# Optimization experiments

Measured on AMD Instinct MI355X. Metric: run time of the kernel, lower is better.

The kernel has to match this reference:

```python
import jax, jax.numpy as jnp
import numpy as np

NH = 12  # num_heads


def _rms(y, g, eps=1e-6):
    # RMSNorm over the full model dim (applied before the head reshape, as in the source)
    return y * jax.lax.rsqrt(jnp.mean(y * y, axis=-1, keepdims=True) + eps) * g


def _rope(t, cos, sin, total_len):
    # t: [B, S, n, d]; rotate first total_len tokens, pass the tail through unchanged
    b, s, n, d = t.shape
    c = d // 2
    tm = t[:, :total_len].reshape(b, total_len, n, c, 2)
    tr, ti = tm[..., 0], tm[..., 1]
    co = cos[None, :, None, :]
    si = sin[None, :, None, :]
    rot = jnp.stack([tr * co - ti * si, tr * si + ti * co], axis=-1).reshape(b, total_len, n, d)
    if total_len < s:
        return jnp.concatenate([rot, t[:, total_len:]], axis=1)
    return rot


def setup_inputs() -> dict:
    key = jax.random.key(0)
    ks = jax.random.split(key, 8)
    B, F, H, W = 4, 4, 16, 28
    S = F * H * W  # 1792 tokens
    D = 1536
    d = D // NH    # 128
    c = d // 2     # 64
    MAXSEQ = 64
    x = jax.random.normal(ks[0], (B, S, D), jnp.float32)
    seq_lens = jnp.full((B,), S, dtype=jnp.int32)
    grid_sizes = jnp.tile(jnp.array([[F, H, W]], dtype=jnp.int32), (B, 1))
    ang = jnp.arange(MAXSEQ, dtype=jnp.float32)[:, None] * (
        10000.0 ** (-jnp.arange(c, dtype=jnp.float32) / c))[None, :]
    w = lambda k, shp: jax.random.normal(k, shp, jnp.float32) * 0.02
    return {
        "x": x,
        "seq_lens": seq_lens,
        "grid_sizes": grid_sizes,
        "freqs_cos": jnp.cos(ang),
        "freqs_sin": jnp.sin(ang),
        "Wq": w(ks[1], (D, D)), "bq": jnp.zeros((D,), jnp.float32),
        "Wk": w(ks[2], (D, D)), "bk": jnp.zeros((D,), jnp.float32),
        "Wv": w(ks[3], (D, D)), "bv": jnp.zeros((D,), jnp.float32),
        "Wo": w(ks[4], (D, D)), "bo": jnp.zeros((D,), jnp.float32),
        "gq": jnp.ones((D,), jnp.float32),
        "gk": jnp.ones((D,), jnp.float32),
        "num_modalities": 1,
    }


def reference(x, seq_lens, grid_sizes, freqs_cos, freqs_sin,
              Wq, bq, Wk, bk, Wv, bv, Wo, bo, gq, gk, num_modalities):
    b, s, D = x.shape
    d = D // NH
    c = d // 2
    # QKV projections + RMSNorm on q/k (norm over the full dim, then split heads)
    q = _rms(x @ Wq.T + bq, gq).reshape(b, s, NH, d)
    k = _rms(x @ Wk.T + bk, gk).reshape(b, s, NH, d)
    v = (x @ Wv.T + bv).reshape(b, s, NH, d)
    # grid metadata is static (same grid for all samples in this setup)
    f, h, w = (int(z) for z in np.asarray(grid_sizes)[0])
    m = int(num_modalities)
    ct = c - 2 * (c // 3)
    ch = c // 3
    seq_per = f * h * w
    total_len = min(seq_per * m, s)

    def grid_freqs(fr):
        # build per-token (t,h,w) frequency table: [seq_per, c], tiled over modalities
        ft = jnp.broadcast_to(fr[:f, :ct][:, None, None, :], (f, h, w, ct))
        fh = jnp.broadcast_to(fr[:h, ct:ct + ch][None, :, None, :], (f, h, w, ch))
        fw = jnp.broadcast_to(fr[:w, ct + ch:c][None, None, :, :], (f, h, w, ch))
        base = jnp.concatenate([ft, fh, fw], axis=-1).reshape(seq_per, c)
        return jnp.tile(base, (m, 1))[:total_len]

    cos = grid_freqs(freqs_cos)
    sin = grid_freqs(freqs_sin)
    q = _rope(q, cos, sin, total_len)
    k = _rope(k, cos, sin, total_len)
    # full (window_size=(-1,-1)) attention with k_lens masking
    scale = 1.0 / jnp.sqrt(jnp.float32(d))
    scores = jnp.einsum('bqhd,bkhd->bhqk', q, k) * scale
    kmask = jnp.arange(s)[None, :] < seq_lens[:, None]  # [B, S]
    scores = jnp.where(kmask[:, None, None, :], scores, jnp.float32(-1e30))
    attn = jax.nn.softmax(scores, axis=-1)
    out = jnp.einsum('bhqk,bkhd->bqhd', attn, v).reshape(b, s, D)
    return out @ Wo.T + bo
```

## Files before the change

kernel.cpp:

```cpp
#include <hip/hip_runtime.h>
#include <hip/hip_bf16.h>

typedef short bf16x8 __attribute__((ext_vector_type(8)));
typedef float f32x4 __attribute__((ext_vector_type(4)));
typedef float f32x16 __attribute__((ext_vector_type(16)));

#define NH 12
#define SEQ 1792
#define DMODEL 1536
#define HD 128

static __device__ __forceinline__ void gload16(const void* g, void* l) {
  __builtin_amdgcn_global_load_lds((const __attribute__((address_space(1))) void*)g,
                                   (__attribute__((address_space(3))) void*)l, 16, 0, 0);
}

static __device__ __forceinline__ short f2bf(float x) {
  __hip_bfloat16 h = __float2bfloat16(x);
  return *reinterpret_cast<short*>(&h);
}

static __device__ __forceinline__ unsigned pack2(float lo, float hi) {
  unsigned a = (unsigned)(unsigned short)f2bf(lo);
  unsigned b = (unsigned)(unsigned short)f2bf(hi);
  return a | (b << 16);
}

__global__ __launch_bounds__(256) void cast_all_kernel(
    const float* __restrict__ x, const float* __restrict__ wq, const float* __restrict__ wk,
    const float* __restrict__ wv, const float* __restrict__ wo,
    __hip_bfloat16* __restrict__ xb, __hip_bfloat16* __restrict__ wb,
    __hip_bfloat16* __restrict__ wob) {
  int i = blockIdx.x * 256 + threadIdx.x;
  const float* src; __hip_bfloat16* dst; int j;
  if (i < 2752512)      { src = x;  dst = xb;            j = i; }
  else if (i < 3342336) { src = wq; dst = wb;            j = i - 2752512; }
  else if (i < 3932160) { src = wk; dst = wb + 2359296;  j = i - 3342336; }
  else if (i < 4521984) { src = wv; dst = wb + 4718592;  j = i - 3932160; }
  else if (i < 5111808) { src = wo; dst = wob;           j = i - 4521984; }
  else return;
  float4 v = reinterpret_cast<const float4*>(src)[j];
  short4 r;
  r.x = f2bf(v.x); r.y = f2bf(v.y); r.z = f2bf(v.z); r.w = f2bf(v.w);
  reinterpret_cast<short4*>(dst)[j] = r;
}

template<int MODE>
__global__ __launch_bounds__(512, 2) void gemm8(
    const __hip_bfloat16* __restrict__ A, const __hip_bfloat16* __restrict__ B,
    int nN, int cpx,
    const float* __restrict__ bq, const float* __restrict__ bk, const float* __restrict__ bv,
    __hip_bfloat16* __restrict__ qbuf, __hip_bfloat16* __restrict__ kbuf,
    __hip_bfloat16* __restrict__ vt,
    const float* __restrict__ bo, float* __restrict__ outp)
{
  constexpr int K = DMODEL;
  constexpr int nT = K / 64;
  constexpr int nIt = nT / 2;
  __shared__ __hip_bfloat16 As[2][2][128 * 64];
  __shared__ __hip_bfloat16 Bs[2][2][128 * 64];
  const int tid = threadIdx.x;
  const int l = tid & 63, w = tid >> 6;
  const int lr = l & 15, lg = l >> 4;
  const int wr = w >> 2, wc = w & 3;

  const int orig = blockIdx.x;
  const int wg = (orig & 7) * cpx + (orig >> 3);
  const int m0 = (wg / nN) * 256, n0 = (wg % nN) * 256;

  const int hrow0 = tid >> 3;
  const int scb0 = ((tid & 7) << 4) ^ ((hrow0 & 7) << 4);

  auto stageA = [&](int t, int half) {
    const char* s = (const char*)(A + (size_t)(m0 + half * 128) * K + t * 64);
    char* d = (char*)&As[t & 1][half][0];
    gload16(s + (size_t)hrow0 * (K * 2) + scb0, d + tid * 16);
    gload16(s + (size_t)(hrow0 + 64) * (K * 2) + scb0, d + (tid + 512) * 16);
  };
  auto stageB = [&](int t, int half) {
    const char* s = (const char*)(B + (size_t)(n0 + half * 128) * K + t * 64);
    char* d = (char*)&Bs[t & 1][half][0];
    gload16(s + (size_t)hrow0 * (K * 2) + scb0, d + tid * 16);
    gload16(s + (size_t)(hrow0 + 64) * (K * 2) + scb0, d + (tid + 512) * 16);
  };

  f32x4 acc[8][4] = {};
  bf16x8 afr[4][2], b0f[2][2], b1f[2][2];

  auto rdA = [&](int par, int mh) {
#pragma unroll
    for (int i = 0; i < 4; ++i) {
      int hrow = (mh * 4 + i) * 16 + lr;
#pragma unroll
      for (int ks = 0; ks < 2; ++ks)
        afr[i][ks] = *reinterpret_cast<const bf16x8*>(
            (const char*)&As[par][wr][0] + hrow * 128 +
            ((ks * 64 + lg * 16) ^ ((hrow & 7) << 4)));
    }
  };
  auto rdB = [&](int par, int nh, bf16x8 (&bqf)[2][2]) {
#pragma unroll
    for (int j = 0; j < 2; ++j) {
      int base = wc * 64 + (nh * 2 + j) * 16;
      int half = base >> 7;
      int hrow = (base & 127) + lr;
#pragma unroll
      for (int ks = 0; ks < 2; ++ks)
        bqf[j][ks] = *reinterpret_cast<const bf16x8*>(
            (const char*)&Bs[par][half][0] + hrow * 128 +
            ((ks * 64 + lg * 16) ^ ((hrow & 7) << 4)));
    }
  };
  auto mf = [&](int mh, int nh, bf16x8 (&bqf)[2][2]) {
    __builtin_amdgcn_s_setprio(1);
#pragma unroll
    for (int i = 0; i < 4; ++i)
#pragma unroll
      for (int j = 0; j < 2; ++j)
#pragma unroll
        for (int ks = 0; ks < 2; ++ks)
          acc[mh * 4 + i][nh * 2 + j] = __builtin_amdgcn_mfma_f32_16x16x32_bf16(
              afr[i][ks], bqf[j][ks], acc[mh * 4 + i][nh * 2 + j], 0, 0, 0);
    __builtin_amdgcn_s_setprio(0);
  };

#define LGKM0 do { asm volatile("s_waitcnt lgkmcnt(0)" ::: "memory"); \
                   __builtin_amdgcn_sched_barrier(0); } while (0)
#define BAR __builtin_amdgcn_s_barrier()

  stageA(0, 0); stageA(0, 1); stageB(0, 0); stageB(0, 1); stageA(1, 0);
  asm volatile("s_waitcnt vmcnt(2)" ::: "memory");
  BAR;

  for (int it = 0; it < nIt; ++it) {
    const int t1 = 2 * it + 1, u0 = 2 * it + 2, u1 = 2 * it + 3;
    rdA(0, 0); rdB(0, 0, b0f);
    stageA(t1, 1);
    LGKM0; mf(0, 0, b0f); BAR;
    rdB(0, 1, b1f);
    stageB(t1, 0);
    LGKM0; mf(0, 1, b1f); BAR;
    rdA(0, 1);
    stageB(t1, 1);
    LGKM0; mf(1, 1, b1f); BAR;
    if (u0 < nT) stageA(u0, 0);
    mf(1, 0, b0f);
    if (it + 1 == nIt) asm volatile("s_waitcnt vmcnt(0)" ::: "memory");
    else               asm volatile("s_waitcnt vmcnt(2)" ::: "memory");
    BAR;
    rdA(1, 0); rdB(1, 0, b0f);
    if (u0 < nT) stageA(u0, 1);
    LGKM0; mf(0, 0, b0f); BAR;
    rdB(1, 1, b1f);
    if (u0 < nT) stageB(u0, 0);
    LGKM0; mf(0, 1, b1f); BAR;
    rdA(1, 1);
    if (u0 < nT) stageB(u0, 1);
    LGKM0; mf(1, 1, b1f); BAR;
    if (u1 < nT) stageA(u1, 0);
    mf(1, 0, b0f);
    asm volatile("s_waitcnt vmcnt(2)" ::: "memory");
    BAR;
  }
#undef LGKM0
#undef BAR

  if (MODE == 0) {
#pragma unroll
    for (int fj = 0; fj < 4; ++fj) {
      int ncol = n0 + wc * 64 + fj * 16 + lr;
      int which = ncol / DMODEL;
      int cc = ncol - which * DMODEL;
      int hh = cc >> 7, dd = cc & 127;
      float bias = (which == 0 ? bq : which == 1 ? bk : bv)[cc];
#pragma unroll
      for (int fi = 0; fi < 8; ++fi)
#pragma unroll
        for (int r = 0; r < 4; ++r) {
          int rowg = m0 + wr * 128 + fi * 16 + lg * 4 + r;
          int bbb = rowg / SEQ;
          int sr = rowg - bbb * SEQ;
          __hip_bfloat16 hv = __float2bfloat16(acc[fi][fj][r] + bias);
          if (which == 0)
            qbuf[(((size_t)(bbb * NH + hh)) * SEQ + sr) * HD + dd] = hv;
          else if (which == 1)
            kbuf[(((size_t)(bbb * NH + hh)) * SEQ + sr) * HD + dd] = hv;
          else
            vt[(((size_t)(bbb * NH + hh)) * HD + dd) * SEQ + sr] = hv;
        }
    }
  } else {
#pragma unroll
    for (int fj = 0; fj < 4; ++fj) {
      int ncol = n0 + wc * 64 + fj * 16 + lr;
      float bias = bo[ncol];
#pragma unroll
      for (int fi = 0; fi < 8; ++fi)
#pragma unroll
        for (int r = 0; r < 4; ++r) {
          int rowg = m0 + wr * 128 + fi * 16 + lg * 4 + r;
          outp[(size_t)rowg * DMODEL + ncol] = acc[fi][fj][r] + bias;
        }
    }
  }
}

__global__ __launch_bounds__(256) void rmsrope_kernel(
    __hip_bfloat16* __restrict__ qb, __hip_bfloat16* __restrict__ kb,
    const float* __restrict__ gq, const float* __restrict__ gk,
    const float* __restrict__ fc, const float* __restrict__ fs,
    const int* __restrict__ gsz, const int* __restrict__ nmod)
{
  const int bs = blockIdx.x;
  const int b = bs / SEQ, s = bs - b * SEQ;
  const int t = threadIdx.x;
  const int f = gsz[0], h = gsz[1], wd = gsz[2];
  const int mm = nmod[0];
  const int seq_per = f * h * wd;
  int total_len = seq_per * mm; if (total_len > SEQ) total_len = SEQ;
  const bool dorope = s < total_len;
  int fi = 0, hi2 = 0, wi = 0;
  if (dorope) {
    int p = s % seq_per;
    fi = p / (h * wd);
    int rem = p - fi * (h * wd);
    hi2 = rem / wd;
    wi = rem - hi2 * wd;
  }
  float qv[3][2], kv[3][2];
  float sq = 0.f, sk = 0.f;
#pragma unroll
  for (int r = 0; r < 3; ++r) {
    int pi = t + r * 256;
    int head = pi >> 6;
    int dd = (pi & 63) * 2;
    size_t addr = (((size_t)(b * NH + head)) * SEQ + s) * HD + dd;
    __hip_bfloat162 q2 = *reinterpret_cast<const __hip_bfloat162*>(&qb[addr]);
    __hip_bfloat162 k2 = *reinterpret_cast<const __hip_bfloat162*>(&kb[addr]);
    qv[r][0] = __bfloat162float(q2.x); qv[r][1] = __bfloat162float(q2.y);
    kv[r][0] = __bfloat162float(k2.x); kv[r][1] = __bfloat162float(k2.y);
    sq += qv[r][0] * qv[r][0] + qv[r][1] * qv[r][1];
    sk += kv[r][0] * kv[r][0] + kv[r][1] * kv[r][1];
  }
#pragma unroll
  for (int off = 1; off < 64; off <<= 1) {
    sq += __shfl_xor(sq, off);
    sk += __shfl_xor(sk, off);
  }
  __shared__ float red[2][4];
  if ((t & 63) == 0) { red[0][t >> 6] = sq; red[1][t >> 6] = sk; }
  __syncthreads();
  float tq = red[0][0] + red[0][1] + red[0][2] + red[0][3];
  float tk = red[1][0] + red[1][1] + red[1][2] + red[1][3];
  float rq = rsqrtf(tq * (1.0f / DMODEL) + 1e-6f);
  float rk = rsqrtf(tk * (1.0f / DMODEL) + 1e-6f);
  const float scale = 0.08838834764831845f;
#pragma unroll
  for (int r = 0; r < 3; ++r) {
    int pi = t + r * 256;
    int head = pi >> 6;
    int dd = (pi & 63) * 2;
    int col = pi * 2;
    size_t addr = (((size_t)(b * NH + head)) * SEQ + s) * HD + dd;
    float q0 = qv[r][0] * rq * gq[col], q1 = qv[r][1] * rq * gq[col + 1];
    float k0 = kv[r][0] * rk * gk[col], k1 = kv[r][1] * rk * gk[col + 1];
    if (dorope) {
      int j = pi & 63;
      int row = (j < 22) ? fi : (j < 43) ? hi2 : wi;
      float co = fc[row * 64 + j], si = fs[row * 64 + j];
      float a;
      a = q0 * co - q1 * si; q1 = q0 * si + q1 * co; q0 = a;
      a = k0 * co - k1 * si; k1 = k0 * si + k1 * co; k0 = a;
    }
    q0 *= scale; q1 *= scale;
    __hip_bfloat162 oq, ok;
    oq.x = __float2bfloat16(q0); oq.y = __float2bfloat16(q1);
    ok.x = __float2bfloat16(k0); ok.y = __float2bfloat16(k1);
    *reinterpret_cast<__hip_bfloat162*>(&qb[addr]) = oq;
    *reinterpret_cast<__hip_bfloat162*>(&kb[addr]) = ok;
  }
}

__global__ __launch_bounds__(256, 2) void attn_kernel(
    const __hip_bfloat16* __restrict__ qb, const __hip_bfloat16* __restrict__ kbuf,
    const __hip_bfloat16* __restrict__ vt, const int* __restrict__ seq_lens,
    __hip_bfloat16* __restrict__ ob)
{
  const int orig = blockIdx.x;
  const int wg = (orig & 7) * 84 + (orig >> 3);
  const int bh = wg / 14, qt = wg % 14;
  const int bbb = bh / NH, hh = bh - bbb * NH;
  const int tid = threadIdx.x;
  const int w = tid >> 6, l = tid & 63;
  const int lq = l & 31, h = l >> 5;
  const int sl = seq_lens[bbb];
  const __hip_bfloat16* Q = qb + (size_t)bh * SEQ * HD;
  const char* Kc = (const char*)(kbuf + (size_t)bh * SEQ * HD);
  const __hip_bfloat16* Vp = vt + (size_t)bh * HD * SEQ;
  const int q0 = qt * 128 + w * 32;

  __shared__ __hip_bfloat16 Kt[2][64 * 128];
  __shared__ __hip_bfloat16 Vt[2][128 * 64];

  bf16x8 qf[8];
#pragma unroll
  for (int kc = 0; kc < 8; ++kc)
    qf[kc] = *reinterpret_cast<const bf16x8*>(
        &Q[(size_t)(q0 + lq) * HD + kc * 16 + h * 8]);

  f32x16 oacc[4] = {};
  float m = -3e38f, ll = 0.f;

  const int nkt = (sl + 63) >> 6;

  auto stageK = [&](int buf, int k0) {
    char* Lb = (char*)&Kt[buf][0];
#pragma unroll
    for (int q2 = 0; q2 < 4; ++q2) {
      int chunk = q2 * 256 + tid;
      int row = chunk >> 4;
      int cb = (chunk & 15) << 4;
      int scb = cb ^ ((row & 7) << 4);
      gload16(Kc + (size_t)(k0 + row) * 256 + scb, Lb + chunk * 16);
    }
  };
  auto stageV = [&](int buf, int k0) {
    char* Lb = (char*)&Vt[buf][0];
#pragma unroll
    for (int q2 = 0; q2 < 4; ++q2) {
      int chunk = q2 * 256 + tid;
      int row = chunk >> 3;
      int cb = (chunk & 7) << 4;
      int scb = cb ^ ((row & 7) << 4);
      gload16(Vp + (size_t)row * SEQ + k0 + (scb >> 1), Lb + chunk * 16);
    }
  };

  stageK(0, 0);
  stageV(0, 0);
  for (int kt = 0; kt < nkt; ++kt) {
    __syncthreads();
    const int k0 = kt * 64;
    if (kt + 1 < nkt) { stageK((kt + 1) & 1, k0 + 64); stageV((kt + 1) & 1, k0 + 64); }
    const char* Kl = (const char*)&Kt[kt & 1][0];
    const char* Vl = (const char*)&Vt[kt & 1][0];

    f32x16 sa[2] = {};
#pragma unroll
    for (int cb = 0; cb < 2; ++cb) {
      int row = cb * 32 + lq;
      int swz = (row & 7) << 4;
#pragma unroll
      for (int kc = 0; kc < 8; ++kc) {
        bf16x8 kf = *reinterpret_cast<const bf16x8*>(
            Kl + row * 256 + ((kc * 32 + h * 16) ^ swz));
        sa[cb] = __builtin_amdgcn_mfma_f32_32x32x16_bf16(kf, qf[kc], sa[cb], 0, 0, 0);
      }
    }

    if (k0 + 64 > sl) {
#pragma unroll
      for (int cb = 0; cb < 2; ++cb)
#pragma unroll
        for (int r = 0; r < 16; ++r) {
          int kg = k0 + cb * 32 + (r & 3) + 8 * (r >> 2) + 4 * h;
          if (kg >= sl) sa[cb][r] = -3e38f;
        }
    }

    float mx = -3e38f;
#pragma unroll
    for (int cb = 0; cb < 2; ++cb)
#pragma unroll
      for (int r = 0; r < 16; ++r) mx = fmaxf(mx, sa[cb][r]);
    mx = fmaxf(mx, __shfl_xor(mx, 32));

    if (__any(mx - m > 8.f)) {
      float mn = fmaxf(m, mx);
      float alpha = __expf(m - mn);
      m = mn;
      ll *= alpha;
#pragma unroll
      for (int r = 0; r < 16; ++r) {
        float ar = __shfl(alpha, (r & 3) + 8 * (r >> 2) + 4 * h);
#pragma unroll
        for (int d0 = 0; d0 < 4; ++d0) oacc[d0][r] *= ar;
      }
    }

    float rs = 0.f;
#pragma unroll
    for (int cb = 0; cb < 2; ++cb)
#pragma unroll
      for (int r = 0; r < 16; ++r) {
        float e = __expf(sa[cb][r] - m);
        sa[cb][r] = e;
        rs += e;
      }
    rs += __shfl_xor(rs, 32);
    ll += rs;

#pragma unroll
    for (int c = 0; c < 4; ++c) {
      const int cb = c >> 1, r0 = 8 * (c & 1);
      unsigned A01 = pack2(sa[cb][r0],     sa[cb][r0 + 1]);
      unsigned A23 = pack2(sa[cb][r0 + 2], sa[cb][r0 + 3]);
      unsigned B01 = pack2(sa[cb][r0 + 4], sa[cb][r0 + 5]);
      unsigned B23 = pack2(sa[cb][r0 + 6], sa[cb][r0 + 7]);
      unsigned s1 = __shfl_xor(h ? A01 : B01, 32);
      unsigned s2 = __shfl_xor(h ? A23 : B23, 32);
      int4 wv;
      wv.x = (int)(h ? s1 : A01);
      wv.y = (int)(h ? s2 : A23);
      wv.z = (int)(h ? B01 : s1);
      wv.w = (int)(h ? B23 : s2);
      bf16x8 pa = *reinterpret_cast<bf16x8*>(&wv);
#pragma unroll
      for (int d0 = 0; d0 < 4; ++d0) {
        int vr = d0 * 32 + lq;
        bf16x8 vv = *reinterpret_cast<const bf16x8*>(
            Vl + vr * 128 + ((c * 32 + h * 16) ^ ((vr & 7) << 4)));
        oacc[d0] = __builtin_amdgcn_mfma_f32_32x32x16_bf16(pa, vv, oacc[d0], 0, 0, 0);
      }
    }
  }

  float invl = 1.0f / ll;
#pragma unroll
  for (int r = 0; r < 16; ++r) {
    int qoff = (r & 3) + 8 * (r >> 2) + 4 * h;
    float ir = __shfl(invl, qoff);
    int qrow = q0 + qoff;
#pragma unroll
    for (int d0 = 0; d0 < 4; ++d0)
      ob[((size_t)bbb * SEQ + qrow) * DMODEL + hh * HD + d0 * 32 + lq] =
          __float2bfloat16(oacc[d0][r] * ir);
  }
}

extern "C" void kernel_launch(void* const* d_in, const int* in_sizes, int n_in,
                              void* d_out, int out_size, void* d_ws, size_t ws_size,
                              hipStream_t stream) {
  const float* x   = (const float*)d_in[0];
  const int* seq_lens   = (const int*)d_in[1];
  const int* grid_sizes = (const int*)d_in[2];
  const float* fc  = (const float*)d_in[3];
  const float* fs  = (const float*)d_in[4];
  const float* Wq  = (const float*)d_in[5];
  const float* bq  = (const float*)d_in[6];
  const float* Wk  = (const float*)d_in[7];
  const float* bk  = (const float*)d_in[8];
  const float* Wv  = (const float*)d_in[9];
  const float* bv  = (const float*)d_in[10];
  const float* Wo  = (const float*)d_in[11];
  const float* bo  = (const float*)d_in[12];
  const float* gq  = (const float*)d_in[13];
  const float* gk  = (const float*)d_in[14];
  const int* nmod  = (const int*)d_in[15];
  float* out = (float*)d_out;

  char* ws = (char*)d_ws;
  __hip_bfloat16* xb   = (__hip_bfloat16*)(ws + 0);
  __hip_bfloat16* wb   = (__hip_bfloat16*)(ws + 22020096);
  __hip_bfloat16* wob  = (__hip_bfloat16*)(ws + 36175872);
  __hip_bfloat16* qbuf = (__hip_bfloat16*)(ws + 40894464);
  __hip_bfloat16* kbuf = (__hip_bfloat16*)(ws + 62914560);
  __hip_bfloat16* vtb  = (__hip_bfloat16*)(ws + 84934656);
  __hip_bfloat16* ob   = xb;

  cast_all_kernel<<<(5111808 + 255) / 256, 256, 0, stream>>>(x, Wq, Wk, Wv, Wo, xb, wb, wob);

  gemm8<0><<<504, 512, 0, stream>>>(xb, wb, 18, 63, bq, bk, bv,
                                    qbuf, kbuf, vtb, nullptr, nullptr);
  rmsrope_kernel<<<7168, 256, 0, stream>>>(qbuf, kbuf, gq, gk, fc, fs, grid_sizes, nmod);
  attn_kernel<<<672, 256, 0, stream>>>(qbuf, kbuf, vtb, seq_lens, ob);
  gemm8<1><<<168, 512, 0, stream>>>(ob, wob, 6, 21, nullptr, nullptr, nullptr,
                                    nullptr, nullptr, nullptr, bo, out);
}
```

Measured before the change: 342.0 us.

## Prefetch next tile's fragments into registers and stage V transpose through LDS

```diff
diff --git a/kernel.cpp b/kernel.cpp
--- a/kernel.cpp
+++ b/kernel.cpp
@@ -57,8 +57,7 @@
   constexpr int K = DMODEL;
   constexpr int nT = K / 64;
   constexpr int nIt = nT / 2;
-  __shared__ __hip_bfloat16 As[2][2][128 * 64];
-  __shared__ __hip_bfloat16 Bs[2][2][128 * 64];
+  __shared__ char LDSRAW[131072];
   const int tid = threadIdx.x;
   const int l = tid & 63, w = tid >> 6;
   const int lr = l & 15, lg = l >> 4;
@@ -73,45 +72,45 @@
 
   auto stageA = [&](int t, int half) {
     const char* s = (const char*)(A + (size_t)(m0 + half * 128) * K + t * 64);
-    char* d = (char*)&As[t & 1][half][0];
+    char* d = LDSRAW + (t & 1) * 32768 + half * 16384;
     gload16(s + (size_t)hrow0 * (K * 2) + scb0, d + tid * 16);
     gload16(s + (size_t)(hrow0 + 64) * (K * 2) + scb0, d + (tid + 512) * 16);
   };
   auto stageB = [&](int t, int half) {
     const char* s = (const char*)(B + (size_t)(n0 + half * 128) * K + t * 64);
-    char* d = (char*)&Bs[t & 1][half][0];
+    char* d = LDSRAW + 65536 + (t & 1) * 32768 + half * 16384;
     gload16(s + (size_t)hrow0 * (K * 2) + scb0, d + tid * 16);
     gload16(s + (size_t)(hrow0 + 64) * (K * 2) + scb0, d + (tid + 512) * 16);
   };
 
   f32x4 acc[8][4] = {};
-  bf16x8 afr[4][2], b0f[2][2], b1f[2][2];
-
-  auto rdA = [&](int par, int mh) {
+  bf16x8 afr0[4][2], afr1[4][2], b0e[2][2], b0o[2][2], b1f[2][2];
+
+  auto RA = [&](int p, int mh, bf16x8 (&dst)[4][2]) {
+    const char* base = LDSRAW + p * 32768 + wr * 16384;
 #pragma unroll
     for (int i = 0; i < 4; ++i) {
       int hrow = (mh * 4 + i) * 16 + lr;
 #pragma unroll
       for (int ks = 0; ks < 2; ++ks)
-        afr[i][ks] = *reinterpret_cast<const bf16x8*>(
-            (const char*)&As[par][wr][0] + hrow * 128 +
-            ((ks * 64 + lg * 16) ^ ((hrow & 7) << 4)));
-    }
-  };
-  auto rdB = [&](int par, int nh, bf16x8 (&bqf)[2][2]) {
+        dst[i][ks] = *reinterpret_cast<const bf16x8*>(
+            base + hrow * 128 + ((ks * 64 + lg * 16) ^ ((hrow & 7) << 4)));
+    }
+  };
+  auto RB = [&](int p, int nh, bf16x8 (&dst)[2][2]) {
 #pragma unroll
     for (int j = 0; j < 2; ++j) {
-      int base = wc * 64 + (nh * 2 + j) * 16;
-      int half = base >> 7;
-      int hrow = (base & 127) + lr;
+      int cbase = wc * 64 + (nh * 2 + j) * 16;
+      int half = cbase >> 7;
+      int hrow = (cbase & 127) + lr;
+      const char* base = LDSRAW + 65536 + p * 32768 + half * 16384;
 #pragma unroll
       for (int ks = 0; ks < 2; ++ks)
-        bqf[j][ks] = *reinterpret_cast<const bf16x8*>(
-            (const char*)&Bs[par][half][0] + hrow * 128 +
-            ((ks * 64 + lg * 16) ^ ((hrow & 7) << 4)));
-    }
-  };
-  auto mf = [&](int mh, int nh, bf16x8 (&bqf)[2][2]) {
+        dst[j][ks] = *reinterpret_cast<const bf16x8*>(
+            base + hrow * 128 + ((ks * 64 + lg * 16) ^ ((hrow & 7) << 4)));
+    }
+  };
+  auto MF = [&](int mh, int nh, bf16x8 (&a)[4][2], bf16x8 (&b)[2][2]) {
     __builtin_amdgcn_s_setprio(1);
 #pragma unroll
     for (int i = 0; i < 4; ++i)
@@ -120,74 +119,106 @@
 #pragma unroll
         for (int ks = 0; ks < 2; ++ks)
           acc[mh * 4 + i][nh * 2 + j] = __builtin_amdgcn_mfma_f32_16x16x32_bf16(
-              afr[i][ks], bqf[j][ks], acc[mh * 4 + i][nh * 2 + j], 0, 0, 0);
+              a[i][ks], b[j][ks], acc[mh * 4 + i][nh * 2 + j], 0, 0, 0);
     __builtin_amdgcn_s_setprio(0);
   };
 
-#define LGKM0 do { asm volatile("s_waitcnt lgkmcnt(0)" ::: "memory"); \
-                   __builtin_amdgcn_sched_barrier(0); } while (0)
+#define SB0 __builtin_amdgcn_sched_barrier(0)
 #define BAR __builtin_amdgcn_s_barrier()
+#define TILE(p, t, b0c, b0n)                                                 \
+  {                               \
+    RB(p, 1, b1f);                                                           \
+    if ((t) + 1 < nT) stageA((t) + 1, 1);                                    \
+    SB0;                                                                     \
+    MF(0, 0, afr0, b0c);                                                     \
+    BAR;                                                                     \
+                                  \
+    RA(p, 1, afr1);                                                          \
+    if ((t) + 1 < nT) stageB((t) + 1, 0);                                    \
+    SB0;                                                                     \
+    MF(0, 1, afr0, b1f);                                                     \
+    BAR;                                                                     \
+                                 \
+    if ((t) + 1 < nT) stageB((t) + 1, 1);                                    \
+    if ((t) + 2 < nT) stageA((t) + 2, 0);                                    \
+    SB0;                                                                     \
+    MF(1, 1, afr1, b1f);                                                     \
+    if ((t) + 2 < nT) asm volatile("s_waitcnt vmcnt(2)" ::: "memory");       \
+    else              asm volatile("s_waitcnt vmcnt(0)" ::: "memory");       \
+    BAR;                                                                     \
+                      \
+    if ((t) + 1 < nT) { RA((p) ^ 1, 0, afr0); RB((p) ^ 1, 0, b0n); }         \
+    SB0;                                                                     \
+    MF(1, 0, afr1, b0c);                                                     \
+    BAR;                                                                     \
+  }
 
   stageA(0, 0); stageA(0, 1); stageB(0, 0); stageB(0, 1); stageA(1, 0);
   asm volatile("s_waitcnt vmcnt(2)" ::: "memory");
   BAR;
-
-  for (int it = 0; it < nIt; ++it) {
-    const int t1 = 2 * it + 1, u0 = 2 * it + 2, u1 = 2 * it + 3;
-    rdA(0, 0); rdB(0, 0, b0f);
-    stageA(t1, 1);
-    LGKM0; mf(0, 0, b0f); BAR;
-    rdB(0, 1, b1f);
-    stageB(t1, 0);
-    LGKM0; mf(0, 1, b1f); BAR;
-    rdA(0, 1);
-    stageB(t1, 1);
-    LGKM0; mf(1, 1, b1f); BAR;
-    if (u0 < nT) stageA(u0, 0);
-    mf(1, 0, b0f);
-    if (it + 1 == nIt) asm volatile("s_waitcnt vmcnt(0)" ::: "memory");
-    else               asm volatile("s_waitcnt vmcnt(2)" ::: "memory");
-    BAR;
-    rdA(1, 0); rdB(1, 0, b0f);
-    if (u0 < nT) stageA(u0, 1);
-    LGKM0; mf(0, 0, b0f); BAR;
-    rdB(1, 1, b1f);
-    if (u0 < nT) stageB(u0, 0);
-    LGKM0; mf(0, 1, b1f); BAR;
-    rdA(1, 1);
-    if (u0 < nT) stageB(u0, 1);
-    LGKM0; mf(1, 1, b1f); BAR;
-    if (u1 < nT) stageA(u1, 0);
-    mf(1, 0, b0f);
-    asm volatile("s_waitcnt vmcnt(2)" ::: "memory");
-    BAR;
-  }
-#undef LGKM0
+  RA(0, 0, afr0); RB(0, 0, b0e);
+
+  for (int it2 = 0; it2 < nIt; ++it2) {
+    TILE(0, 2 * it2, b0e, b0o);
+    TILE(1, 2 * it2 + 1, b0o, b0e);
+  }
+#undef TILE
+#undef SB0
 #undef BAR
 
   if (MODE == 0) {
-#pragma unroll
-    for (int fj = 0; fj < 4; ++fj) {
-      int ncol = n0 + wc * 64 + fj * 16 + lr;
-      int which = ncol / DMODEL;
-      int cc = ncol - which * DMODEL;
-      int hh = cc >> 7, dd = cc & 127;
-      float bias = (which == 0 ? bq : which == 1 ? bk : bv)[cc];
-#pragma unroll
-      for (int fi = 0; fi < 8; ++fi)
-#pragma unroll
-        for (int r = 0; r < 4; ++r) {
-          int rowg = m0 + wr * 128 + fi * 16 + lg * 4 + r;
-          int bbb = rowg / SEQ;
-          int sr = rowg - bbb * SEQ;
-          __hip_bfloat16 hv = __float2bfloat16(acc[fi][fj][r] + bias);
-          if (which == 0)
-            qbuf[(((size_t)(bbb * NH + hh)) * SEQ + sr) * HD + dd] = hv;
-          else if (which == 1)
-            kbuf[(((size_t)(bbb * NH + hh)) * SEQ + sr) * HD + dd] = hv;
-          else
-            vt[(((size_t)(bbb * NH + hh)) * HD + dd) * SEQ + sr] = hv;
-        }
+    const int which = n0 / DMODEL;
+    if (which < 2) {
+#pragma unroll
+      for (int fj = 0; fj < 4; ++fj) {
+        int ncol = n0 + wc * 64 + fj * 16 + lr;
+        int cc = ncol - which * DMODEL;
+        int hh = cc >> 7, dd = cc & 127;
+        float bias = (which == 0 ? bq : bk)[cc];
+#pragma unroll
+        for (int fi = 0; fi < 8; ++fi)
+#pragma unroll
+          for (int r = 0; r < 4; ++r) {
+            int rowg = m0 + wr * 128 + fi * 16 + lg * 4 + r;
+            int bbb = rowg / SEQ;
+            int sr = rowg - bbb * SEQ;
+            __hip_bfloat16 hv = __float2bfloat16(acc[fi][fj][r] + bias);
+            if (which == 0)
+              qbuf[(((size_t)(bbb * NH + hh)) * SEQ + sr) * HD + dd] = hv;
+            else
+              kbuf[(((size_t)(bbb * NH + hh)) * SEQ + sr) * HD + dd] = hv;
+          }
+      }
+    } else {
+      __syncthreads();
+      const int cc0 = n0 - 2 * DMODEL;
+#pragma unroll
+      for (int fj = 0; fj < 4; ++fj) {
+        int d_loc = wc * 64 + fj * 16 + lr;
+        float bias = bv[cc0 + d_loc];
+#pragma unroll
+        for (int fi = 0; fi < 8; ++fi)
+#pragma unroll
+          for (int r = 0; r < 4; ++r) {
+            int s_loc = wr * 128 + fi * 16 + lg * 4 + r;
+            *reinterpret_cast<short*>(LDSRAW + d_loc * 512 +
+                ((s_loc * 2) ^ ((d_loc & 7) << 4))) = f2bf(acc[fi][fj][r] + bias);
+          }
+      }
+      __syncthreads();
+      const int bbb = m0 / SEQ;
+      const int sr0 = m0 - bbb * SEQ;
+#pragma unroll
+      for (int c = 0; c < 16; ++c) {
+        int g = c * 512 + tid;
+        int d = g >> 5;
+        int sb = (g & 31) << 4;
+        bf16x8 vvv = *reinterpret_cast<const bf16x8*>(
+            LDSRAW + d * 512 + (sb ^ ((d & 7) << 4)));
+        int ddg = cc0 + d, hh = ddg >> 7, dd = ddg & 127;
+        *reinterpret_cast<bf16x8*>(
+            &vt[(((size_t)(bbb * NH + hh)) * HD + dd) * SEQ + sr0 + (sb >> 1)]) = vvv;
+      }
     }
   } else {
 #pragma unroll
```

New measurement: 326.8 us. 4.5% less time.
